# Kernel tuning notes

Measured on AMD Instinct MI355X. Metric: run time of the kernel, lower is better.

Reference implementation:

```python
import jax, jax.numpy as jnp
import numpy as np

B, T, D = 2, 1024, 1024
NH, HD = 16, 64          # attention heads, head dim (D = NH*HD)
M = 16                   # LRU block size
H = D // M               # number of LRU blocks = 64
EPS = 1e-5
ROPE_BASE = 10000.0


def rmsnorm(x, w):
    ms = jnp.mean(x * x, axis=-1, keepdims=True)
    return x * jax.lax.rsqrt(ms + EPS) * w


def rope_tables(t_len, dtype):
    inv_freq = 1.0 / (ROPE_BASE ** (jnp.arange(0, HD, 2, dtype=jnp.float32) / HD))
    freqs = jnp.arange(t_len, dtype=jnp.float32)[:, None] * inv_freq[None, :]  # [T, HD/2]
    emb = jnp.concatenate([freqs, freqs], axis=-1)                              # [T, HD]
    return emb.astype(dtype)


def apply_rope(x, emb):
    # x: [B, T, NH, HD]
    cos = jnp.cos(emb)[None, :, None, :]
    sin = jnp.sin(emb)[None, :, None, :]
    x1, x2 = jnp.split(x, 2, axis=-1)
    return x * cos + jnp.concatenate([-x2, x1], axis=-1) * sin


def setup_inputs() -> dict:
    key = jax.random.key(0)
    ks = jax.random.split(key, 7)
    w = lambda k, shape: jax.random.normal(k, shape, dtype=jnp.float32) * 0.02
    return {
        "x": jax.random.normal(ks[0], (B, T, D), dtype=jnp.float32),
        "attn_norm_w": jnp.ones((D,), jnp.float32),
        "w_qkv": w(ks[1], (D, 3 * D)),
        "w_attn_out": w(ks[2], (D, D)),
        "lru_norm_w": jnp.ones((D,), jnp.float32),
        "w_v": w(ks[3], (D, D)),
        "w_a": w(ks[4], (D, H * M * (M + 1))),
        "w_out_proj": w(ks[5], (D, D)),
    }


def reference(x, attn_norm_w, w_qkv, w_attn_out, lru_norm_w, w_v, w_a, w_out_proj):
    # ---- RoPE causal attention block (residual) ----
    h = rmsnorm(x, attn_norm_w)
    qkv = (h @ w_qkv).reshape(B, T, 3, NH, HD)
    q, k, v = qkv[:, :, 0], qkv[:, :, 1], qkv[:, :, 2]
    emb = rope_tables(T, x.dtype)
    q = apply_rope(q, emb)
    k = apply_rope(k, emb)
    scores = jnp.einsum("bthd,bshd->bhts", q, k) / jnp.sqrt(jnp.asarray(HD, x.dtype))
    causal = jnp.tril(jnp.ones((T, T), dtype=bool))
    scores = jnp.where(causal[None, None], scores, jnp.asarray(-1e30, x.dtype))
    attn = jax.nn.softmax(scores, axis=-1)
    o = jnp.einsum("bhts,bshd->bthd", attn, v).reshape(B, T, D)
    x = x + o @ w_attn_out

    # ---- BlockDiagonalLRU block (residual) ----
    h2 = rmsnorm(x, lru_norm_w)
    vv = (h2 @ w_v).reshape(B, T, H, M)
    gates = jax.nn.softmax((h2 @ w_a).reshape(B, T, H, M, M + 1), axis=-1)
    a0 = gates[..., 0]   # [B, T, H, M]
    A = gates[..., 1:]   # [B, T, H, M, M]

    def step(state, inp):
        A_t, a0_t, v_t = inp  # [B,H,M,M], [B,H,M], [B,H,M]
        new = jnp.einsum("bhij,bhj->bhi", A_t, state) + a0_t * v_t
        return new, new

    init = jnp.zeros((B, H, M), x.dtype)
    _, outs = jax.lax.scan(
        step, init,
        (jnp.moveaxis(A, 1, 0), jnp.moveaxis(a0, 1, 0), jnp.moveaxis(vv, 1, 0)),
    )
    h_out = jnp.moveaxis(outs, 0, 1).reshape(B, T, D)
    return x + h_out @ w_out_proj
```

## Files before the change

kernel.cpp:

```cpp
#include <hip/hip_runtime.h>


typedef unsigned short u16;
typedef unsigned int   u32;
typedef __bf16 bf16x8 __attribute__((ext_vector_type(8)));
typedef float  f32x4  __attribute__((ext_vector_type(4)));

#define B_  2
#define T_  1024
#define D_  1024
#define NH_ 16
#define HD_ 64
#define H_  64
#define M_  16

__device__ __forceinline__ float b2f(u16 u) {
    return __uint_as_float(((u32)u) << 16);
}
__device__ __forceinline__ u16 f2b(float f) {
    u32 u = __float_as_uint(f);
    u32 r = (u + 0x7FFFu + ((u >> 16) & 1u)) >> 16;
    return (u16)r;
}
__device__ __forceinline__ float blo(u32 u) { return __uint_as_float(u << 16); }
__device__ __forceinline__ float bhi(u32 u) { return __uint_as_float(u & 0xFFFF0000u); }

__device__ __forceinline__ void stage16(const void* gp, void* lp) {
    typedef __attribute__((address_space(1))) const unsigned int GU;
    typedef __attribute__((address_space(3))) unsigned int LU;
    __builtin_amdgcn_global_load_lds((GU*)gp, (LU*)lp, 16, 0, 0);
}

template<int BM, int BN, int BK, int MODE, bool TRUNCK, bool CAUSAL, int SWZ>
__global__ __launch_bounds__(256) void gemm_bt(
    const u16* __restrict__ A, const u16* __restrict__ Bt,
    void* __restrict__ Cout, void* __restrict__ Cout2, void* __restrict__ Cout3,
    const float* __restrict__ addend,
    int M, int N, int K, long strideA, long strideB, long strideC)
{
    constexpr int MT = BM / 32;
    constexpr int NT = BN / 32;
    constexpr int KCH = BK / 8;
    const int z  = blockIdx.z;
    int bx = blockIdx.x, by = blockIdx.y;
    if (SWZ == 2) {
        int f = by * gridDim.x + bx;
        int xcd = f & 7, k = f >> 3;
        by = k & 15;
        bx = xcd * (gridDim.x >> 3) + (k >> 4);
    }
    const int m0 = by * BM;
    const int n0 = bx * BN;
    if (CAUSAL && n0 > m0 + BM - 1) return;
    const int Keff = TRUNCK ? (K < m0 + BM ? K : m0 + BM) : K;

    const u16* Ab = A  + (size_t)z * (size_t)strideA;
    const u16* Bb = Bt + (size_t)z * (size_t)strideB;

    __shared__ alignas(16) u16 As[BM * BK];
    __shared__ alignas(16) u16 Bs[BN * BK];

    const int tid  = threadIdx.x;
    const int lane = tid & 63, w = tid >> 6;
    const int wr = w >> 1, wc = w & 1;
    const int quad = lane >> 4, l16 = lane & 15;

    f32x4 acc[MT][NT] = {};

    constexpr int AITER = (BM * BK / 8) / 256;
    constexpr int BITER = (BN * BK / 8) / 256;

    for (int k0 = 0; k0 < Keff; k0 += BK) {
        #pragma unroll
        for (int it = 0; it < AITER; ++it) {
            int c = it * 256 + tid;
            int m = c / KCH, kc = c % KCH;
            stage16(Ab + (size_t)(m0 + m) * K + k0 + kc * 8,
                    &As[(it * 256 + w * 64) * 8]);
        }
        #pragma unroll
        for (int it = 0; it < BITER; ++it) {
            int c = it * 256 + tid;
            int n = c / KCH, kc = c % KCH;
            stage16(Bb + (size_t)(n0 + n) * K + k0 + kc * 8,
                    &Bs[(it * 256 + w * 64) * 8]);
        }
        __syncthreads();

        #pragma unroll
        for (int kk = 0; kk < BK; kk += 32) {
            bf16x8 af[MT], bfr[NT];
            #pragma unroll
            for (int mt = 0; mt < MT; ++mt)
                af[mt] = *(const bf16x8*)&As[(wr * (BM / 2) + mt * 16 + l16) * BK + kk + quad * 8];
            #pragma unroll
            for (int nt = 0; nt < NT; ++nt)
                bfr[nt] = *(const bf16x8*)&Bs[(wc * (BN / 2) + nt * 16 + l16) * BK + kk + quad * 8];
            #pragma unroll
            for (int mt = 0; mt < MT; ++mt)
                #pragma unroll
                for (int nt = 0; nt < NT; ++nt)
                    acc[mt][nt] = __builtin_amdgcn_mfma_f32_16x16x32_bf16(
                        af[mt], bfr[nt], acc[mt][nt], 0, 0, 0);
        }
        __syncthreads();
    }

    if (MODE == 6) {
        const int reg = n0 >> 10;
        const int hh  = ((n0 & 1023) >> 6) + wc;
        #pragma unroll
        for (int mt = 0; mt < MT; ++mt) {
            #pragma unroll
            for (int r = 0; r < 4; ++r) {
                int row = m0 + wr * (BM / 2) + mt * 16 + quad * 4 + r;
                int t = row & (T_ - 1), bb = row >> 10;
                size_t obase = ((size_t)(bb * NH_ + hh) * T_ + t) * HD_;
                if (reg == 2) {
                    #pragma unroll
                    for (int nt = 0; nt < 4; ++nt)
                        ((u16*)Cout3)[obase + nt * 16 + l16] = f2b(acc[mt][nt][r]);
                } else {
                    u16* dst = (reg == 0) ? (u16*)Cout : (u16*)Cout2;
                    #pragma unroll
                    for (int nt = 0; nt < 2; ++nt) {
                        int i = nt * 16 + l16;
                        float ang = (float)t * exp2f(-(float)i * 0.41524101186092034f);
                        float sn, cs;
                        sincosf(ang, &sn, &cs);
                        float q1 = acc[mt][nt][r], q2 = acc[mt][nt + 2][r];
                        dst[obase + i]      = f2b(q1 * cs - q2 * sn);
                        dst[obase + i + 32] = f2b(q2 * cs + q1 * sn);
                    }
                }
            }
        }
        return;
    }
    #pragma unroll
    for (int mt = 0; mt < MT; ++mt) {
        #pragma unroll
        for (int nt = 0; nt < NT; ++nt) {
            #pragma unroll
            for (int r = 0; r < 4; ++r) {
                int row = m0 + wr * (BM / 2) + mt * 16 + quad * 4 + r;
                int col = n0 + wc * (BN / 2) + nt * 16 + l16;
                float val = acc[mt][nt][r];
                if (MODE == 0) {
                    if (addend) val += addend[(size_t)row * N + col];
                    ((float*)Cout)[(size_t)z * (size_t)strideC + (size_t)row * N + col] = val;
                } else if (MODE == 1) {
                    ((u16*)Cout)[(size_t)z * (size_t)strideC + (size_t)row * N + col] = f2b(val);
                } else if (MODE == 2) {
                    size_t idx = ((size_t)(z >> 4) * T_ + row) * (size_t)D_ + (z & 15) * HD_ + col;
                    ((u16*)Cout)[idx] = f2b(val);
                }
            }
        }
    }
}

__global__ __launch_bounds__(256, 3) void gemm_gates128(
    const u16* __restrict__ A, const u16* __restrict__ Bt,
    u16* __restrict__ gates, float* __restrict__ vvT)
{
    constexpr int K = 1024;
    constexpr int NTILE = 16;

    const int f = blockIdx.y * gridDim.x + blockIdx.x;
    const int xcd = f & 7, k8 = f >> 3;
    const int by = k8 & 15;
    const int bx = xcd * 12 + (k8 >> 4);
    const int m0 = by * 128;
    const int n0 = bx * 192;

    __shared__ alignas(16) u16 As[128 * 64];
    __shared__ alignas(16) u16 Bs[192 * 64];

    const int tid  = threadIdx.x;
    const int lane = tid & 63, w = tid >> 6;
    const int wr = w >> 1, wc = w & 1;
    const int quad = lane >> 4, l16 = lane & 15;

    const int colOff = (((tid & 7) ^ ((tid >> 3) & 7)) * 8);
    const u16* pA = A  + (size_t)(m0 + (tid >> 3)) * K + colOff;
    const u16* pB = Bt + (size_t)(n0 + (tid >> 3)) * K + colOff;
    const int wbase = w * 512;

    const int sq0 = quad ^ (l16 & 7);
    const int sq1 = sq0 ^ 4;
    const int aoff0 = (wr * 64 + l16) * 64 + sq0 * 8;
    const int aoff1 = (wr * 64 + l16) * 64 + sq1 * 8;
    const int boff0 = (wc * 96 + l16) * 64 + sq0 * 8;
    const int boff1 = (wc * 96 + l16) * 64 + sq1 * 8;

    f32x4 acc[4][6] = {};

    #pragma unroll 1
    for (int t = 0; t < NTILE; ++t) {
        const int kc = t * 64;
        #pragma unroll
        for (int c = 0; c < 4; ++c)
            stage16(pA + (size_t)(c * 32) * K + kc, &As[c * 2048 + wbase]);
        #pragma unroll
        for (int c = 0; c < 6; ++c)
            stage16(pB + (size_t)(c * 32) * K + kc, &Bs[c * 2048 + wbase]);
        __syncthreads();

        bf16x8 af[4], bfr[6];
        #pragma unroll
        for (int mt = 0; mt < 4; ++mt) af[mt]  = *(const bf16x8*)&As[aoff0 + mt * 1024];
        #pragma unroll
        for (int nt = 0; nt < 6; ++nt) bfr[nt] = *(const bf16x8*)&Bs[boff0 + nt * 1024];
        #pragma unroll
        for (int mt = 0; mt < 4; ++mt)
            #pragma unroll
            for (int nt = 0; nt < 6; ++nt)
                acc[mt][nt] = __builtin_amdgcn_mfma_f32_16x16x32_bf16(
                    af[mt], bfr[nt], acc[mt][nt], 0, 0, 0);
        #pragma unroll
        for (int mt = 0; mt < 4; ++mt) af[mt]  = *(const bf16x8*)&As[aoff1 + mt * 1024];
        #pragma unroll
        for (int nt = 0; nt < 6; ++nt) bfr[nt] = *(const bf16x8*)&Bs[boff1 + nt * 1024];
        #pragma unroll
        for (int mt = 0; mt < 4; ++mt)
            #pragma unroll
            for (int nt = 0; nt < 6; ++nt)
                acc[mt][nt] = __builtin_amdgcn_mfma_f32_16x16x32_bf16(
                    af[mt], bfr[nt], acc[mt][nt], 0, 0, 0);
        __syncthreads();
    }

    const int cgbase = bx * 12 + wc * 6;
    #pragma unroll
    for (int mt = 0; mt < 4; ++mt) {
        #pragma unroll
        for (int r = 0; r < 4; ++r) {
            int row = m0 + wr * 64 + mt * 16 + quad * 4 + r;
            int tt = row & (T_ - 1), bb = row >> 10;
            #pragma unroll
            for (int nt = 0; nt < 6; ++nt) {
                int cg = cgbase + nt;
                float val = acc[mt][nt][r];
                if (cg >= 1088) {
                    vvT[(((size_t)(bb * 64 + (cg - 1088))) * T_ + tt) * 16 + l16] = val;
                } else {
                    int hh = cg / 17, rem = cg - hh * 17;
                    gates[(((size_t)(bb * 64 + hh)) * T_ + tt) * 272 + rem * 16 + l16] = f2b(val);
                }
            }
        }
    }
}

__global__ __launch_bounds__(256) void rmsnorm_k(
    const float* __restrict__ x, const float* __restrict__ w, u16* __restrict__ out)
{
    const int row = blockIdx.x, tid = threadIdx.x;
    float4 v = ((const float4*)(x + (size_t)row * D_))[tid];
    float ss = v.x * v.x + v.y * v.y + v.z * v.z + v.w * v.w;
    #pragma unroll
    for (int o = 32; o >= 1; o >>= 1) ss += __shfl_xor(ss, o, 64);
    __shared__ float red[4];
    if ((tid & 63) == 0) red[tid >> 6] = ss;
    __syncthreads();
    ss = red[0] + red[1] + red[2] + red[3];
    float scale = rsqrtf(ss * (1.0f / D_) + 1e-5f);
    float4 wv = ((const float4*)w)[tid];
    ushort4 o4;
    o4.x = f2b(v.x * scale * wv.x);
    o4.y = f2b(v.y * scale * wv.y);
    o4.z = f2b(v.z * scale * wv.z);
    o4.w = f2b(v.w * scale * wv.w);
    ((ushort4*)(out + (size_t)row * D_))[tid] = o4;
}

__global__ void convT_all(
    const float* __restrict__ wqkv, const float* __restrict__ wao,
    const float* __restrict__ wv,   const float* __restrict__ wa,
    const float* __restrict__ wop,
    u16* __restrict__ wqkvT, u16* __restrict__ waoT,
    u16* __restrict__ waT,   u16* __restrict__ wopT)
{
    const int x = blockIdx.x;
    const float* in; u16* out; int C, xb;
    if (x < 96)       { in = wqkv; out = wqkvT; C = 3072;  xb = x; }
    else if (x < 128) { in = wao;  out = waoT;  C = 1024;  xb = x - 96; }
    else if (x < 160) { in = wv;   out = waT + (size_t)17408 * 1024; C = 1024; xb = x - 128; }
    else if (x < 704) { in = wa;   out = waT;   C = 17408; xb = x - 160; }
    else              { in = wop;  out = wopT;  C = 1024;  xb = x - 704; }
    constexpr int R = 1024;
    __shared__ float tile[32][33];
    const int c0 = xb * 32, r0 = blockIdx.y * 32;
    const int tx = threadIdx.x, ty = threadIdx.y;
    #pragma unroll
    for (int k = 0; k < 4; ++k)
        tile[ty + 8 * k][tx] = in[(size_t)(r0 + ty + 8 * k) * C + c0 + tx];
    __syncthreads();
    #pragma unroll
    for (int k = 0; k < 4; ++k)
        out[(size_t)(c0 + ty + 8 * k) * R + r0 + tx] = f2b(tile[tx][ty + 8 * k]);
}

__global__ void transpose_bf16_k(const u16* __restrict__ in_, u16* __restrict__ out_, int R, int C)
{
    __shared__ u16 tile[32][33];
    const u16* in = in_ + (size_t)blockIdx.z * R * C;
    u16* out      = out_ + (size_t)blockIdx.z * R * C;
    const int c0 = blockIdx.x * 32, r0 = blockIdx.y * 32;
    const int tx = threadIdx.x, ty = threadIdx.y;
    #pragma unroll
    for (int k = 0; k < 4; ++k)
        tile[ty + 8 * k][tx] = in[(size_t)(r0 + ty + 8 * k) * C + c0 + tx];
    __syncthreads();
    #pragma unroll
    for (int k = 0; k < 4; ++k)
        out[(size_t)(c0 + ty + 8 * k) * R + r0 + tx] = tile[tx][ty + 8 * k];
}

__global__ __launch_bounds__(256) void softmax_causal_k(u16* __restrict__ S)
{
    const int w = threadIdx.x >> 6, lane = threadIdx.x & 63;
    const int z = blockIdx.x * 4 + w;
    const int t = z & (T_ - 1);
    u16* row = S + (size_t)z * T_;
    const int n = t + 1;
    const int kmax = (t & ~63) + 64;
    const int kb = lane * 4;
    float v[4][4];
    float mx = -1e30f;
    #pragma unroll
    for (int it = 0; it < 4; ++it) {
        int k = it * 256 + kb;
        if (k < kmax) {
            uint2 d = *(const uint2*)(row + k);
            v[it][0] = (k + 0 < n) ? blo(d.x) * 0.125f : -1e30f;
            v[it][1] = (k + 1 < n) ? bhi(d.x) * 0.125f : -1e30f;
            v[it][2] = (k + 2 < n) ? blo(d.y) * 0.125f : -1e30f;
            v[it][3] = (k + 3 < n) ? bhi(d.y) * 0.125f : -1e30f;
        } else {
            v[it][0] = v[it][1] = v[it][2] = v[it][3] = -1e30f;
        }
        mx = fmaxf(mx, fmaxf(fmaxf(v[it][0], v[it][1]), fmaxf(v[it][2], v[it][3])));
    }
    #pragma unroll
    for (int o = 32; o >= 1; o >>= 1) mx = fmaxf(mx, __shfl_xor(mx, o, 64));
    float sum = 0.f;
    #pragma unroll
    for (int it = 0; it < 4; ++it)
        #pragma unroll
        for (int j = 0; j < 4; ++j) {
            float e = (v[it][j] > -1e29f) ? __expf(v[it][j] - mx) : 0.f;
            v[it][j] = e;
            sum += e;
        }
    #pragma unroll
    for (int o = 32; o >= 1; o >>= 1) sum += __shfl_xor(sum, o, 64);
    float inv = 1.0f / sum;
    #pragma unroll
    for (int it = 0; it < 4; ++it) {
        int k = it * 256 + kb;
        if (k < kmax) {
            uint2 d;
            d.x = (u32)f2b(v[it][0] * inv) | ((u32)f2b(v[it][1] * inv) << 16);
            d.y = (u32)f2b(v[it][2] * inv) | ((u32)f2b(v[it][3] * inv) << 16);
            *(uint2*)(row + k) = d;
        }
    }
}

__device__ __forceinline__ void scan_prep(u16* glds, float* vlds, int lane)
{
    #pragma unroll
    for (int rnd = 0; rnd < 2; ++rnd) {
        float p[4][17];
        #pragma unroll
        for (int j = 0; j < 4; ++j) {
            int r = rnd * 256 + j * 64 + lane;
            const u16* g = &glds[r * 17];
            float vv[17];
            float mx = -1e30f;
            #pragma unroll
            for (int tt = 0; tt < 17; ++tt) { vv[tt] = b2f(g[tt]); mx = fmaxf(mx, vv[tt]); }
            float s = 0.f;
            #pragma unroll
            for (int tt = 0; tt < 17; ++tt) { vv[tt] = __expf(vv[tt] - mx); s += vv[tt]; }
            float inv = 1.0f / s;
            #pragma unroll
            for (int tt = 0; tt < 17; ++tt) p[j][tt] = vv[tt] * inv;
        }
        __syncthreads();
        #pragma unroll
        for (int j = 0; j < 4; ++j) {
            int r = rnd * 256 + j * 64 + lane;
            uint4 w0, w1;
            w0.x = (u32)f2b(p[j][1])  | ((u32)f2b(p[j][2])  << 16);
            w0.y = (u32)f2b(p[j][3])  | ((u32)f2b(p[j][4])  << 16);
            w0.z = (u32)f2b(p[j][5])  | ((u32)f2b(p[j][6])  << 16);
            w0.w = (u32)f2b(p[j][7])  | ((u32)f2b(p[j][8])  << 16);
            w1.x = (u32)f2b(p[j][9])  | ((u32)f2b(p[j][10]) << 16);
            w1.y = (u32)f2b(p[j][11]) | ((u32)f2b(p[j][12]) << 16);
            w1.z = (u32)f2b(p[j][13]) | ((u32)f2b(p[j][14]) << 16);
            w1.w = (u32)f2b(p[j][15]) | ((u32)f2b(p[j][16]) << 16);
            ((uint4*)glds)[r * 2]     = w0;
            ((uint4*)glds)[r * 2 + 1] = w1;
            vlds[r] *= p[j][0];
        }
        __syncthreads();
    }
}

__global__ __launch_bounds__(64) void scan_p1(
    const u16* __restrict__ gates, const float* __restrict__ vvT,
    float* __restrict__ Pmat, float* __restrict__ evec)
{
    const int c = blockIdx.x, chain = blockIdx.y;
    const int lane = threadIdx.x;
    const int i = lane >> 2, q = lane & 3;
    __shared__ alignas(16) u16   glds[32 * 272];
    __shared__ alignas(16) float vlds[32 * 16];
    __shared__ alignas(16) float Pb[2][256];
    __shared__ float slds[16];

    const char* gbase = (const char*)(gates + ((size_t)chain * T_ + c * 32) * 272);
    #pragma unroll
    for (int it = 0; it < 17; ++it)
        stage16(gbase + it * 1024 + lane * 16, (char*)glds + it * 1024);
    const char* vbase = (const char*)(vvT + ((size_t)chain * T_ + c * 32) * 16);
    #pragma unroll
    for (int it = 0; it < 2; ++it)
        stage16(vbase + it * 1024 + lane * 16, (char*)vlds + it * 1024);
    __syncthreads();

    scan_prep(glds, vlds, lane);

    {
        f32x4 idq;
        #pragma unroll
        for (int m = 0; m < 4; ++m) idq[m] = (i == q * 4 + m) ? 1.f : 0.f;
        *(f32x4*)&Pb[0][i * 16 + q * 4] = idq;
    }
    f32x4 e4[4] = {};
    f32x4 np = {};
    float neLast = 0.f;
    int cur = 0;

    for (int st = 0; st < 32; ++st) {
        const uint4* rp = (const uint4*)((const char*)glds + (st * 16 + i) * 32);
        uint4 d0 = rp[0], d1 = rp[1];
        float ar[16];
        ar[0]  = blo(d0.x); ar[1]  = bhi(d0.x);
        ar[2]  = blo(d0.y); ar[3]  = bhi(d0.y);
        ar[4]  = blo(d0.z); ar[5]  = bhi(d0.z);
        ar[6]  = blo(d0.w); ar[7]  = bhi(d0.w);
        ar[8]  = blo(d1.x); ar[9]  = bhi(d1.x);
        ar[10] = blo(d1.y); ar[11] = bhi(d1.y);
        ar[12] = blo(d1.z); ar[13] = bhi(d1.z);
        ar[14] = blo(d1.w); ar[15] = bhi(d1.w);

        f32x4 pk[16];
        #pragma unroll
        for (int k = 0; k < 16; ++k)
            pk[k] = *(const f32x4*)&Pb[cur][k * 16 + q * 4];

        f32x4 a = pk[0] * ar[0];
        #pragma unroll
        for (int k = 1; k < 16; ++k) a += pk[k] * ar[k];
        np = a;

        float ne0 = ar[0] * e4[0][0] + ar[1] * e4[0][1] + ar[2] * e4[0][2] + ar[3] * e4[0][3];
        float ne1 = ar[4] * e4[1][0] + ar[5] * e4[1][1] + ar[6] * e4[1][2] + ar[7] * e4[1][3];
        float ne2 = ar[8] * e4[2][0] + ar[9] * e4[2][1] + ar[10] * e4[2][2] + ar[11] * e4[2][3];
        float ne3 = ar[12] * e4[3][0] + ar[13] * e4[3][1] + ar[14] * e4[3][2] + ar[15] * e4[3][3];
        float ne = (ne0 + ne1) + (ne2 + ne3) + vlds[st * 16 + i];

        *(f32x4*)&Pb[cur ^ 1][i * 16 + q * 4] = np;
        if (q == 0) slds[i] = ne;
        #pragma unroll
        for (int m = 0; m < 4; ++m) e4[m] = *(const f32x4*)&slds[m * 4];
        neLast = ne;
        cur ^= 1;
    }

    float* Pd = Pmat + ((size_t)chain * 32 + c) * 256;
    *(f32x4*)&Pd[i * 16 + q * 4] = np;
    if (q == 0) evec[((size_t)chain * 32 + c) * 16 + i] = neLast;
}

__global__ __launch_bounds__(64) void scan_comb(
    const float* __restrict__ Pmat, const float* __restrict__ evec, float* __restrict__ sIn)
{
    const int chain = blockIdx.x;
    const int lane = threadIdx.x;
    const int i = lane >> 2, q = lane & 3;
    __shared__ alignas(16) float Pl[32 * 256];
    __shared__ alignas(16) float El[32 * 16];
    __shared__ float slds[16];

    const char* Pg = (const char*)(Pmat + (size_t)chain * 32 * 256);
    #pragma unroll
    for (int it = 0; it < 32; ++it)
        stage16(Pg + it * 1024 + lane * 16, (char*)Pl + it * 1024);
    const char* Eg = (const char*)(evec + (size_t)chain * 32 * 16);
    #pragma unroll
    for (int it = 0; it < 2; ++it)
        stage16(Eg + it * 1024 + lane * 16, (char*)El + it * 1024);
    __syncthreads();

    f32x4 s4[4] = {};
    if (q == 0) sIn[((size_t)chain * 32 + 0) * 16 + i] = 0.f;
    for (int cc = 0; cc < 32; ++cc) {
        f32x4 pr[4];
        #pragma unroll
        for (int m = 0; m < 4; ++m)
            pr[m] = *(const f32x4*)&Pl[cc * 256 + i * 16 + m * 4];
        float ne = 0.f;
        #pragma unroll
        for (int k = 0; k < 16; ++k) ne += pr[k >> 2][k & 3] * s4[k >> 2][k & 3];
        ne += El[cc * 16 + i];
        if (q == 0) {
            slds[i] = ne;
            if (cc < 31) sIn[((size_t)chain * 32 + cc + 1) * 16 + i] = ne;
        }
        #pragma unroll
        for (int m = 0; m < 4; ++m) s4[m] = *(const f32x4*)&slds[m * 4];
    }
}

__global__ __launch_bounds__(64) void scan_p2(
    const u16* __restrict__ gates, const float* __restrict__ vvT,
    const float* __restrict__ sIn, u16* __restrict__ hout)
{
    const int c = blockIdx.x, chain = blockIdx.y;
    const int b = chain >> 6, hh = chain & 63;
    const int lane = threadIdx.x;
    const int i = lane >> 2, q = lane & 3;
    __shared__ alignas(16) u16   glds[32 * 272];
    __shared__ alignas(16) float vlds[32 * 16];
    __shared__ float slds[16];

    const char* gbase = (const char*)(gates + ((size_t)chain * T_ + c * 32) * 272);
    #pragma unroll
    for (int it = 0; it < 17; ++it)
        stage16(gbase + it * 1024 + lane * 16, (char*)glds + it * 1024);
    const char* vbase = (const char*)(vvT + ((size_t)chain * T_ + c * 32) * 16);
    #pragma unroll
    for (int it = 0; it < 2; ++it)
        stage16(vbase + it * 1024 + lane * 16, (char*)vlds + it * 1024);
    __syncthreads();

    scan_prep(glds, vlds, lane);

    const float* sp = sIn + ((size_t)chain * 32 + c) * 16;
    f32x4 s4[4];
    #pragma unroll
    for (int m = 0; m < 4; ++m) s4[m] = *(const f32x4*)(sp + m * 4);

    u16* hbase = hout + ((size_t)(b * T_ + c * 32)) * D_ + hh * 16;
    for (int st = 0; st < 32; ++st) {
        const uint4* rp = (const uint4*)((const char*)glds + (st * 16 + i) * 32);
        uint4 d0 = rp[0], d1 = rp[1];
        float ne0 = blo(d0.x) * s4[0][0] + bhi(d0.x) * s4[0][1]
                  + blo(d0.y) * s4[0][2] + bhi(d0.y) * s4[0][3];
        float ne1 = blo(d0.z) * s4[1][0] + bhi(d0.z) * s4[1][1]
                  + blo(d0.w) * s4[1][2] + bhi(d0.w) * s4[1][3];
        float ne2 = blo(d1.x) * s4[2][0] + bhi(d1.x) * s4[2][1]
                  + blo(d1.y) * s4[2][2] + bhi(d1.y) * s4[2][3];
        float ne3 = blo(d1.z) * s4[3][0] + bhi(d1.z) * s4[3][1]
                  + blo(d1.w) * s4[3][2] + bhi(d1.w) * s4[3][3];
        float ne = (ne0 + ne1) + (ne2 + ne3) + vlds[st * 16 + i];
        if (q == 0) {
            slds[i] = ne;
            hbase[(size_t)st * D_ + i] = f2b(ne);
        }
        #pragma unroll
        for (int m = 0; m < 4; ++m) s4[m] = *(const f32x4*)&slds[m * 4];
    }
}

extern "C" void kernel_launch(void* const* d_in, const int* in_sizes, int n_in,
                              void* d_out, int out_size, void* d_ws, size_t ws_size,
                              hipStream_t stream)
{
    const float* x    = (const float*)d_in[0];
    const float* anw  = (const float*)d_in[1];
    const float* wqkv = (const float*)d_in[2];
    const float* wao  = (const float*)d_in[3];
    const float* lnw  = (const float*)d_in[4];
    const float* wv   = (const float*)d_in[5];
    const float* wa   = (const float*)d_in[6];
    const float* wop  = (const float*)d_in[7];

    char* ws = (char*)d_ws;
    const size_t MB = 1u << 20;
    u16*   h     = (u16*)  (ws +   0 * MB);
    u16*   h2    = (u16*)  (ws +   4 * MB);
    u16*   wqkvT = (u16*)  (ws +   8 * MB);
    u16*   waoT  = (u16*)  (ws +  14 * MB);
    u16*   wopT  = (u16*)  (ws +  16 * MB);
    u16*   waT   = (u16*)  (ws +  18 * MB);
    float* x2    = (float*)(ws +  54 * MB);
    float* vvT   = (float*)(ws +  62 * MB);
    u16*   Qb    = (u16*)  (ws +  78 * MB);
    float* Pmat  = (float*)(ws +  78 * MB);
    u16*   Kb    = (u16*)  (ws +  82 * MB);
    float* evec  = (float*)(ws +  82 * MB);
    float* sIn   = (float*)(ws +  82 * MB + 256 * 1024);
    u16*   Vb    = (u16*)  (ws +  86 * MB);
    u16*   Vt    = (u16*)  (ws +  90 * MB);
    u16*   S     = (u16*)  (ws +  94 * MB);
    u16*   omat  = (u16*)  (ws + 158 * MB);
    u16*   gates = (u16*)  (ws +  94 * MB);
    u16*   hout  = (u16*)  (ws + 162 * MB);
    (void)in_sizes; (void)n_in; (void)out_size; (void)ws_size;

    dim3 tb(32, 8);
    convT_all<<<dim3(736, 32), tb, 0, stream>>>(
        wqkv, wao, wv, wa, wop, wqkvT, waoT, waT, wopT);

    rmsnorm_k<<<2048, 256, 0, stream>>>(x, anw, h);
    gemm_bt<64, 128, 32, 6, false, false, 0><<<dim3(24, 32, 1), 256, 0, stream>>>(
        h, wqkvT, (void*)Qb, (void*)Kb, (void*)Vb, nullptr, 2048, 3072, 1024, 0, 0, 0);
    transpose_bf16_k<<<dim3(2, 32, 32), tb, 0, stream>>>(Vb, Vt, 1024, 64);

    gemm_bt<128, 128, 64, 1, false, true, 0><<<dim3(8, 8, 32), 256, 0, stream>>>(
        Qb, Kb, (void*)S, nullptr, nullptr, nullptr, 1024, 1024, 64, 65536, 65536, 1048576);
    softmax_causal_k<<<8192, 256, 0, stream>>>(S);
    gemm_bt<64, 64, 64, 2, true, false, 0><<<dim3(1, 16, 32), 256, 0, stream>>>(
        S, Vt, (void*)omat, nullptr, nullptr, nullptr, 1024, 64, 1024, 1048576, 65536, 0);

    gemm_bt<64, 128, 32, 0, false, false, 0><<<dim3(8, 32, 1), 256, 0, stream>>>(
        omat, waoT, (void*)x2, nullptr, nullptr, x, 2048, 1024, 1024, 0, 0, 0);
    rmsnorm_k<<<2048, 256, 0, stream>>>(x2, lnw, h2);

    gemm_gates128<<<dim3(96, 16), 256, 0, stream>>>(h2, waT, gates, vvT);

    scan_p1<<<dim3(32, 128), 64, 0, stream>>>(gates, vvT, Pmat, evec);
    scan_comb<<<128, 64, 0, stream>>>(Pmat, evec, sIn);
    scan_p2<<<dim3(32, 128), 64, 0, stream>>>(gates, vvT, sIn, hout);

    gemm_bt<64, 128, 32, 0, false, false, 0><<<dim3(8, 32, 1), 256, 0, stream>>>(
        hout, wopT, d_out, nullptr, nullptr, x2, 2048, 1024, 1024, 0, 0, 0);
}
```

Measured before the change: 478.6 us.

## Fuse causal attention into a single flash-attention kernel with online softmax

Replaces the three-kernel attention path (QK^T GEMM writing a full bf16 score matrix, a separate causal softmax pass, then the PV GEMM) with one flash-style kernel. Each block handles a 64-row query tile, loops over causal key tiles only, and keeps a running max/sum so no score matrix is written to global memory. This removes about 64MB of score-matrix traffic and two kernel launches. In exchange it serializes work per query tile, and only 512 blocks of uneven length run, paired in an attempt to balance the causal workload.

```diff
diff --git a/kernel.cpp b/kernel.cpp
--- a/kernel.cpp
+++ b/kernel.cpp
@@ -160,6 +160,159 @@
     }
 }
 
+__global__ __launch_bounds__(256) void attn_flash(
+    const u16* __restrict__ Qb, const u16* __restrict__ Kb,
+    const u16* __restrict__ Vt, u16* __restrict__ omat)
+{
+    const int f = blockIdx.x;
+    const int u = f & 255, rr2 = f >> 8;
+    const int z  = (rr2 == 0) ? (u >> 4) : 16 + (u >> 4);
+    const int qb = (rr2 == 0) ? (u & 15) : 15 - (u & 15);
+
+    const u16* Qz = Qb + (size_t)z * 65536;
+    const u16* Kz = Kb + (size_t)z * 65536;
+    const u16* Vz = Vt + (size_t)z * 65536;
+
+    __shared__ alignas(16) u16 Qs[64 * 64];
+    __shared__ alignas(16) u16 Ks[64 * 64];
+    __shared__ alignas(16) u16 Vs[64 * 64];
+    __shared__ alignas(16) u16 Ps[4][16 * 64];
+
+    const int tid  = threadIdx.x;
+    const int lane = tid & 63, w = tid >> 6;
+    const int quad = lane >> 4, l16 = lane & 15;
+
+    const int srow   = tid >> 3;
+    const int colOff = (((tid & 7) ^ (srow & 7)) * 8);
+    const int wbase  = w * 512;
+
+    #pragma unroll
+    for (int c = 0; c < 2; ++c)
+        stage16(Qz + (size_t)(qb * 64 + c * 32 + srow) * 64 + colOff,
+                &Qs[c * 2048 + wbase]);
+    __syncthreads();
+
+    const int qrow = w * 16 + l16;
+    bf16x8 qf[2];
+    #pragma unroll
+    for (int ks = 0; ks < 2; ++ks)
+        qf[ks] = *(const bf16x8*)&Qs[qrow * 64 + (((ks * 4 + quad) ^ (l16 & 7)) * 8)];
+
+    f32x4 acc_o[4] = {};
+    float m_run = -1e30f, l_run = 0.f;
+
+    const int sq0 = (quad ^ (l16 & 7)) * 8;
+    const int sq1 = ((4 + quad) ^ (l16 & 7)) * 8;
+
+    u16* Pw = &Ps[w][0];
+    int pwa[4];
+    #pragma unroll
+    for (int mt = 0; mt < 4; ++mt) {
+        int g = mt * 4 + quad;
+        pwa[mt] = l16 * 64 + (((g >> 1) ^ (l16 & 7)) * 8) + (g & 1) * 4;
+    }
+
+    for (int kt = 0; kt <= qb; ++kt) {
+        __syncthreads();
+        #pragma unroll
+        for (int c = 0; c < 2; ++c)
+            stage16(Kz + (size_t)(kt * 64 + c * 32 + srow) * 64 + colOff,
+                    &Ks[c * 2048 + wbase]);
+        #pragma unroll
+        for (int c = 0; c < 2; ++c)
+            stage16(Vz + (size_t)(c * 32 + srow) * 1024 + kt * 64 + colOff,
+                    &Vs[c * 2048 + wbase]);
+        __syncthreads();
+
+        f32x4 accs[4] = {};
+        #pragma unroll
+        for (int ks = 0; ks < 2; ++ks) {
+            const int so = ks ? sq1 : sq0;
+            bf16x8 af[4];
+            #pragma unroll
+            for (int mt = 0; mt < 4; ++mt)
+                af[mt] = *(const bf16x8*)&Ks[(mt * 16 + l16) * 64 + so];
+            #pragma unroll
+            for (int mt = 0; mt < 4; ++mt)
+                accs[mt] = __builtin_amdgcn_mfma_f32_16x16x32_bf16(
+                    af[mt], qf[ks], accs[mt], 0, 0, 0);
+        }
+
+        float sv[4][4];
+        float mx = -1e30f;
+        const bool diag = (kt == qb);
+        #pragma unroll
+        for (int mt = 0; mt < 4; ++mt)
+            #pragma unroll
+            for (int r = 0; r < 4; ++r) {
+                int kv = mt * 16 + quad * 4 + r;
+                float s = accs[mt][r] * 0.125f;
+                if (diag && kv > qrow) s = -1e30f;
+                sv[mt][r] = s;
+                mx = fmaxf(mx, s);
+            }
+        mx = fmaxf(mx, __shfl_xor(mx, 16, 64));
+        mx = fmaxf(mx, __shfl_xor(mx, 32, 64));
+
+        const float m_new = fmaxf(m_run, mx);
+        const float sc    = __expf(m_run - m_new);
+
+        float tsum = 0.f;
+        u16 pb[4][4];
+        #pragma unroll
+        for (int mt = 0; mt < 4; ++mt)
+            #pragma unroll
+            for (int r = 0; r < 4; ++r) {
+                float p = (sv[mt][r] > -1e29f) ? __expf(sv[mt][r] - m_new) : 0.f;
+                tsum += p;
+                pb[mt][r] = f2b(p);
+            }
+        tsum += __shfl_xor(tsum, 16, 64);
+        tsum += __shfl_xor(tsum, 32, 64);
+        l_run = l_run * sc + tsum;
+        m_run = m_new;
+
+        #pragma unroll
+        for (int mt = 0; mt < 4; ++mt) {
+            ushort4 pk = { pb[mt][0], pb[mt][1], pb[mt][2], pb[mt][3] };
+            *(ushort4*)&Pw[pwa[mt]] = pk;
+        }
+
+        #pragma unroll
+        for (int r = 0; r < 4; ++r) {
+            float scr = __shfl(sc, quad * 4 + r, 64);
+            #pragma unroll
+            for (int nt = 0; nt < 4; ++nt) acc_o[nt][r] *= scr;
+        }
+
+        #pragma unroll
+        for (int ks = 0; ks < 2; ++ks) {
+            const int so = ks ? sq1 : sq0;
+            bf16x8 pf = *(const bf16x8*)&Pw[l16 * 64 + so];
+            bf16x8 vf[4];
+            #pragma unroll
+            for (int nt = 0; nt < 4; ++nt)
+                vf[nt] = *(const bf16x8*)&Vs[(nt * 16 + l16) * 64 + so];
+            #pragma unroll
+            for (int nt = 0; nt < 4; ++nt)
+                acc_o[nt] = __builtin_amdgcn_mfma_f32_16x16x32_bf16(
+                    pf, vf[nt], acc_o[nt], 0, 0, 0);
+        }
+    }
+
+    const float linv = 1.0f / l_run;
+    const int qg0 = qb * 64 + w * 16;
+    #pragma unroll
+    for (int r = 0; r < 4; ++r) {
+        float li = __shfl(linv, quad * 4 + r, 64);
+        int row = qg0 + quad * 4 + r;
+        size_t obase = ((size_t)(z >> 4) * T_ + row) * D_ + (z & 15) * HD_;
+        #pragma unroll
+        for (int nt = 0; nt < 4; ++nt)
+            omat[obase + nt * 16 + l16] = f2b(acc_o[nt][r] * li);
+    }
+}
+
 __global__ __launch_bounds__(256, 3) void gemm_gates128(
     const u16* __restrict__ A, const u16* __restrict__ Bt,
     u16* __restrict__ gates, float* __restrict__ vvT)
@@ -316,57 +469,6 @@
     #pragma unroll
     for (int k = 0; k < 4; ++k)
         out[(size_t)(c0 + ty + 8 * k) * R + r0 + tx] = tile[tx][ty + 8 * k];
-}
-
-__global__ __launch_bounds__(256) void softmax_causal_k(u16* __restrict__ S)
-{
-    const int w = threadIdx.x >> 6, lane = threadIdx.x & 63;
-    const int z = blockIdx.x * 4 + w;
-    const int t = z & (T_ - 1);
-    u16* row = S + (size_t)z * T_;
-    const int n = t + 1;
-    const int kmax = (t & ~63) + 64;
-    const int kb = lane * 4;
-    float v[4][4];
-    float mx = -1e30f;
-    #pragma unroll
-    for (int it = 0; it < 4; ++it) {
-        int k = it * 256 + kb;
-        if (k < kmax) {
-            uint2 d = *(const uint2*)(row + k);
-            v[it][0] = (k + 0 < n) ? blo(d.x) * 0.125f : -1e30f;
-            v[it][1] = (k + 1 < n) ? bhi(d.x) * 0.125f : -1e30f;
-            v[it][2] = (k + 2 < n) ? blo(d.y) * 0.125f : -1e30f;
-            v[it][3] = (k + 3 < n) ? bhi(d.y) * 0.125f : -1e30f;
-        } else {
-            v[it][0] = v[it][1] = v[it][2] = v[it][3] = -1e30f;
-        }
-        mx = fmaxf(mx, fmaxf(fmaxf(v[it][0], v[it][1]), fmaxf(v[it][2], v[it][3])));
-    }
-    #pragma unroll
-    for (int o = 32; o >= 1; o >>= 1) mx = fmaxf(mx, __shfl_xor(mx, o, 64));
-    float sum = 0.f;
-    #pragma unroll
-    for (int it = 0; it < 4; ++it)
-        #pragma unroll
-        for (int j = 0; j < 4; ++j) {
-            float e = (v[it][j] > -1e29f) ? __expf(v[it][j] - mx) : 0.f;
-            v[it][j] = e;
-            sum += e;
-        }
-    #pragma unroll
-    for (int o = 32; o >= 1; o >>= 1) sum += __shfl_xor(sum, o, 64);
-    float inv = 1.0f / sum;
-    #pragma unroll
-    for (int it = 0; it < 4; ++it) {
-        int k = it * 256 + kb;
-        if (k < kmax) {
-            uint2 d;
-            d.x = (u32)f2b(v[it][0] * inv) | ((u32)f2b(v[it][1] * inv) << 16);
-            d.y = (u32)f2b(v[it][2] * inv) | ((u32)f2b(v[it][3] * inv) << 16);
-            *(uint2*)(row + k) = d;
-        }
-    }
 }
 
 __device__ __forceinline__ void scan_prep(u16* glds, float* vlds, int lane)
@@ -608,7 +710,6 @@
     float* sIn   = (float*)(ws +  82 * MB + 256 * 1024);
     u16*   Vb    = (u16*)  (ws +  86 * MB);
     u16*   Vt    = (u16*)  (ws +  90 * MB);
-    u16*   S     = (u16*)  (ws +  94 * MB);
     u16*   omat  = (u16*)  (ws + 158 * MB);
     u16*   gates = (u16*)  (ws +  94 * MB);
     u16*   hout  = (u16*)  (ws + 162 * MB);
@@ -623,11 +724,7 @@
         h, wqkvT, (void*)Qb, (void*)Kb, (void*)Vb, nullptr, 2048, 3072, 1024, 0, 0, 0);
     transpose_bf16_k<<<dim3(2, 32, 32), tb, 0, stream>>>(Vb, Vt, 1024, 64);
 
-    gemm_bt<128, 128, 64, 1, false, true, 0><<<dim3(8, 8, 32), 256, 0, stream>>>(
-        Qb, Kb, (void*)S, nullptr, nullptr, nullptr, 1024, 1024, 64, 65536, 65536, 1048576);
-    softmax_causal_k<<<8192, 256, 0, stream>>>(S);
-    gemm_bt<64, 64, 64, 2, true, false, 0><<<dim3(1, 16, 32), 256, 0, stream>>>(
-        S, Vt, (void*)omat, nullptr, nullptr, nullptr, 1024, 64, 1024, 1048576, 65536, 0);
+    attn_flash<<<512, 256, 0, stream>>>(Qb, Kb, Vt, omat);
 
     gemm_bt<64, 128, 32, 0, false, false, 0><<<dim3(8, 32, 1), 256, 0, stream>>>(
         omat, waoT, (void*)x2, nullptr, nullptr, x, 2048, 1024, 1024, 0, 0, 0);
```

Measured after the change: 454.6 us. -5.0%, faster.
